# Kernel optimization log

Hardware: AMD Instinct MI355X
Metric: run time of the kernel (lower is better)

The kernel has to match this reference:

```python
import jax, jax.numpy as jnp
import numpy as np

# Config (matches init_kwargs)
T, B = 128, 32
I, H, O, G = 128, 320, 32, 8
GROUP = 16  # attn_group_size entries, 8 groups of 16 -> sums to I
DT, TAU_X, TAU_W = 0.02, 0.1, 0.2
ALPHA_X = DT / TAU_X          # 0.2
ALPHA_W = DT / TAU_W          # 0.1
E_PROP = 0.8


def _masks():
    e_h = int(E_PROP * H)  # 256
    # x2h: e_prop=1, zero_cols_prop=0, no diag removal -> all ones
    mask_x = jnp.ones((H, I), dtype=jnp.float32)
    # h2h: sign mask (+1 for E, -1 for I), diagonal zeroed
    sign_h = jnp.concatenate([jnp.ones(e_h), -jnp.ones(H - e_h)]).astype(jnp.float32)
    mask_h = jnp.tile(sign_h[None, :], (H, 1)) * (1.0 - jnp.eye(H, dtype=jnp.float32))
    # h2o: zero_cols = int(0.2*H) trailing columns removed, sign mask on the rest
    zc = int((1.0 - E_PROP) * H)  # 64
    exist = jnp.concatenate([jnp.ones(H - zc), jnp.zeros(zc)]).astype(jnp.float32)
    mask_o = jnp.tile((sign_h * exist)[None, :], (O, 1))
    # attn EILinear(H -> G): same column pattern as h2o
    mask_a = jnp.tile((sign_h * exist)[None, :], (G, 1))
    return mask_x, mask_h, mask_o, mask_a


def setup_inputs() -> dict:
    key = jax.random.key(0)
    ks = jax.random.split(key, 10)
    s = 0.05  # keep dynamics in a sane range
    return {
        "x": jax.random.normal(ks[0], (T, B, I), dtype=jnp.float32),
        "Rs": jax.random.uniform(ks[1], (T, B, 1), dtype=jnp.float32),
        "W_x2h": jax.random.normal(ks[2], (H, I), dtype=jnp.float32) * s,
        "W_h2h": jax.random.normal(ks[3], (H, H), dtype=jnp.float32) * s,
        "b_h2h": jax.random.normal(ks[4], (H,), dtype=jnp.float32) * s,
        "W_h2o": jax.random.normal(ks[5], (O, H), dtype=jnp.float32) * s,
        "b_h2o": jax.random.normal(ks[6], (O,), dtype=jnp.float32) * s,
        "W_attn": jax.random.normal(ks[7], (G, H), dtype=jnp.float32) * s,
        "b_attn": jax.random.normal(ks[8], (G,), dtype=jnp.float32) * s,
        "c_plas": jax.random.normal(ks[9], (6,), dtype=jnp.float32) * s,
    }


def reference(x, Rs, W_x2h, W_h2h, b_h2h, W_h2o, b_h2o, W_attn, b_attn, c_plas):
    mask_x, mask_h, mask_o, mask_a = _masks()
    relu = jax.nn.relu
    # effective (sign/existence constrained, positive) weights
    ew_attn = relu(W_attn) * mask_a                      # [G, H]
    ew_x0 = relu(W_x2h) * mask_x                         # [H, I]
    ew_h0 = relu(W_h2h) * mask_h                         # [H, H]
    c = jnp.abs(c_plas)

    state0 = jnp.zeros((B, H), dtype=x.dtype)            # x0=0, sigma_rec=0
    output0 = relu(state0)
    wx0 = jnp.broadcast_to(ew_x0[None], (B, H, I))       # batched fast weights
    wh0 = jnp.broadcast_to(ew_h0[None], (B, H, H))

    def step(carry, inp):
        state, output, wx, wh = carry
        x_t, R_t = inp                                   # [B,I], [B,1]
        # attention over hidden groups
        attn = jax.nn.softmax(output @ ew_attn.T + b_attn, axis=-1)  # [B,G]
        attn_full = jnp.repeat(attn, GROUP, axis=-1)     # [B,I]
        xm = x_t * attn_full * G
        # masked / positive-constrained fast weights applied per batch
        ewx = relu(wx) * mask_x[None]                    # [B,H,I]
        ewh = relu(wh) * mask_h[None]                    # [B,H,H]
        total = (jnp.einsum('bhi,bi->bh', ewx, xm)
                 + jnp.einsum('bhj,bj->bh', ewh, output) + b_h2h)
        new_state = state * (1.0 - ALPHA_X) + total * ALPHA_X
        new_output = jnp.tanh(relu(new_state))           # retanh
        # outer-product plasticity update
        R = R_t[:, :, None]                              # [B,1,1]
        wx_n = wx * (1.0 - ALPHA_W) + ALPHA_W * R * (
            c[0] * xm[:, None, :]
            + c[1] * new_output[:, :, None]
            + c[2] * jnp.einsum('bi,bj->bij', new_output, xm))
        wh_n = wh * (1.0 - ALPHA_W) + ALPHA_W * R * (
            c[3] * output[:, None, :]
            + c[4] * new_output[:, :, None]
            + c[5] * jnp.einsum('bi,bj->bij', new_output, output))
        return (new_state, new_output, wx_n, wh_n), new_output

    _, hs = jax.lax.scan(step, (state0, output0, wx0, wh0), (x, Rs))  # hs: [T,B,H]
    ew_o = relu(W_h2o) * mask_o                          # [O,H]
    out = jax.nn.sigmoid(jnp.einsum('tbh,oh->tbo', hs, ew_o) + b_h2o)
    return out, hs
```

## Files before the change

kernel.cpp:

```cpp
#include <hip/hip_runtime.h>

#define TT 128
#define BB 32
#define II 128
#define HH 320
#define OO 32
#define GG 8
#define HPAD 129

static __device__ __forceinline__ float fexp2(float x) { return __builtin_amdgcn_exp2f(x); }
static __device__ __forceinline__ float frcp(float x)  { return __builtin_amdgcn_rcpf(x); }

static __device__ __forceinline__ float tanh_pos(float x) {
    float e = fexp2(x * 2.8853900817779268f);
    return 1.0f - 2.0f * frcp(e + 1.0f);
}

__global__ __launch_bounds__(512, 2)
void leaky_rnn_kernel(const float* __restrict__ x, const float* __restrict__ Rs,
                      const float* __restrict__ Wx2h, const float* __restrict__ Wh2h,
                      const float* __restrict__ bh2h, const float* __restrict__ Wh2o,
                      const float* __restrict__ bh2o, const float* __restrict__ Wattn,
                      const float* __restrict__ battn, const float* __restrict__ cplas,
                      float* __restrict__ out, float* __restrict__ hs,
                      unsigned* __restrict__ ctr)
{
    const int tid  = threadIdx.x;
    const int bid  = blockIdx.x;
    const int b    = bid >> 3;
    const int sub  = bid & 7;
    const int w    = tid >> 6;
    const int lane = tid & 63;
    const int h0   = sub * 40;

    __shared__ float s_ea[GG * HH];
    __shared__ float s_out[HH];
    __shared__ float s_xm[II];
    __shared__ float s_logit[GG];
    __shared__ float s_hist[40 * HPAD];
    __shared__ float s_hs[16 * HH];

    for (int idx = tid; idx < GG * HH; idx += 512) {
        int h = idx % HH;
        float m = (h < 256) ? 1.f : (h == 256 ? -1.f : 0.f);
        s_ea[idx] = fmaxf(Wattn[idx], 0.f) * m;
    }
    if (tid < HH) s_out[tid] = 0.f;

    float wx[5][2], wh[5][5], st[5], bh[5];
    int hrow[5];
#pragma unroll
    for (int r = 0; r < 5; ++r) {
        int h = h0 + w * 5 + r;
        hrow[r] = h;
        bh[r] = bh2h[h];
        st[r] = 0.f;
#pragma unroll
        for (int c = 0; c < 2; ++c)
            wx[r][c] = fmaxf(Wx2h[h * II + lane + 64 * c], 0.f);
#pragma unroll
        for (int c = 0; c < 5; ++c) {
            int j = lane + 64 * c;
            float v = fmaxf(Wh2h[h * HH + j], 0.f);
            v = (c == 4) ? -v : v;
            wh[r][c] = (j == h) ? 0.f : v;
        }
    }
    float batt = battn[w];
    float c0 = fabsf(cplas[0]), c1 = fabsf(cplas[1]), c2 = fabsf(cplas[2]);
    float c3 = fabsf(cplas[3]), c4 = fabsf(cplas[4]), c5 = fabsf(cplas[5]);

    const float AX  = (float)(0.02 / 0.1);
    const float AW  = (float)(0.02 / 0.2);
    const float OMX = 1.f - AX;
    const float OMW = 1.f - AW;
    const float L2E = 1.4426950408889634f;

    __syncthreads();

    float xv_next = (tid < II) ? x[b * II + tid] : 0.f;

#pragma unroll 1
    for (int t = 0; t < TT; ++t) {
        float xv = xv_next;
        float Rv = Rs[t * BB + b];
        float A  = AW * Rv;

        float lp = 0.f;
#pragma unroll
        for (int k = 0; k < 5; ++k) {
            int hh2 = lane + 64 * k;
            lp = fmaf(s_ea[w * HH + hh2], s_out[hh2], lp);
        }
#pragma unroll
        for (int m = 1; m < 64; m <<= 1) lp += __shfl_xor(lp, m, 64);
        if (lane == 0) s_logit[w] = lp + batt;
        __syncthreads();

        if (tid < II) {
            float lg[8];
#pragma unroll
            for (int g = 0; g < 8; ++g) lg[g] = s_logit[g];
            float mx = lg[0];
#pragma unroll
            for (int g = 1; g < 8; ++g) mx = fmaxf(mx, lg[g]);
            float se = 0.f, eg[8];
#pragma unroll
            for (int g = 0; g < 8; ++g) { eg[g] = fexp2((lg[g] - mx) * L2E); se += eg[g]; }
            s_xm[tid] = xv * eg[tid >> 4] * 8.f * frcp(se);
        }
        __syncthreads();

        float xmc0 = s_xm[lane], xmc1 = s_xm[lane + 64];
        float oc[5];
#pragma unroll
        for (int c = 0; c < 5; ++c) oc[c] = s_out[lane + 64 * c];

        float no[5];
#pragma unroll
        for (int r = 0; r < 5; ++r) {
            int h = hrow[r];
            float p = fmaxf(wx[r][0], 0.f) * xmc0;
            p = fmaf(fmaxf(wx[r][1], 0.f), xmc1, p);
#pragma unroll
            for (int c = 0; c < 5; ++c) {
                float wv = fmaxf(wh[r][c], 0.f);
                float so = (c == 4) ? -oc[4] : oc[c];
                float term = wv * so;
                term = ((lane + 64 * c) == h) ? 0.f : term;
                p += term;
            }
#pragma unroll
            for (int m = 1; m < 64; m <<= 1) p += __shfl_xor(p, m, 64);
            float total = p + bh[r];
            st[r] = fmaf(st[r], OMX, total * AX);
            no[r] = tanh_pos(fmaxf(st[r], 0.f));
            if (lane == r) {
                __hip_atomic_store(&hs[(t * BB + b) * HH + h], no[r] + 2.0f,
                                   __ATOMIC_RELAXED, __HIP_MEMORY_SCOPE_AGENT);
                s_hist[(w * 5 + r) * HPAD + t] = no[r];
            }
        }

        if (t < TT - 1) {
            float Ac0 = A * c0, Ac1 = A * c1, Ac2 = A * c2;
            float Ac3 = A * c3, Ac4 = A * c4, Ac5 = A * c5;
#pragma unroll
            for (int r = 0; r < 5; ++r) {
                float u  = fmaf(Ac2, no[r], Ac0);
                float v  = Ac1 * no[r];
                float pp = fmaf(Ac5, no[r], Ac3);
                float qq = Ac4 * no[r];
                wx[r][0] = fmaf(wx[r][0], OMW, fmaf(u, xmc0, v));
                wx[r][1] = fmaf(wx[r][1], OMW, fmaf(u, xmc1, v));
#pragma unroll
                for (int c = 0; c < 5; ++c)
                    wh[r][c] = fmaf(wh[r][c], OMW, fmaf(pp, oc[c], qq));
            }
        }

        if (t + 1 < TT)
            xv_next = (tid < II) ? x[((t + 1) * BB + b) * II + tid] : 0.f;

        __syncthreads();

        if (t < TT - 1 && tid < HH) {
            float v;
            if (tid >= h0 && tid < h0 + 40) {
                v = s_hist[(tid - h0) * HPAD + t];
            } else {
                int guard = 0;
                do {
                    v = __hip_atomic_load(&hs[(t * BB + b) * HH + tid],
                                          __ATOMIC_RELAXED, __HIP_MEMORY_SCOPE_AGENT);
                    if (++guard > 2000000) break;
                } while (v < 1.0f);
                v -= 2.0f;
            }
            s_out[tid] = v;
        }
        __syncthreads();
    }

    if (tid == 0) {
        __hip_atomic_fetch_add(&ctr[b * 32], 1u, __ATOMIC_RELAXED, __HIP_MEMORY_SCOPE_AGENT);
        int guard = 0;
        while (__hip_atomic_load(&ctr[b * 32], __ATOMIC_RELAXED, __HIP_MEMORY_SCOPE_AGENT) < 8u) {
            if (++guard > 2000000) break;
            __builtin_amdgcn_s_sleep(1);
        }
    }
    __syncthreads();

    for (int idx = tid; idx < 16 * HH; idx += 512) {
        int tl = idx / HH, h = idx % HH;
        int t_g = sub * 16 + tl;
        s_hs[idx] = __hip_atomic_load(&hs[(t_g * BB + b) * HH + h],
                                      __ATOMIC_RELAXED, __HIP_MEMORY_SCOPE_AGENT) - 2.0f;
    }
    __syncthreads();
    {
        int t_loc = tid >> 5;
        int o     = tid & 31;
        int t_g   = sub * 16 + t_loc;
        const float* hp = &s_hs[t_loc * HH];
        float acc = bh2o[o];
#pragma unroll 4
        for (int h = 0; h < 257; ++h) {
            float m = (h == 256) ? -1.f : 1.f;
            acc = fmaf(fmaxf(Wh2o[o * HH + h], 0.f) * m, hp[h], acc);
        }
        float sg = frcp(1.f + fexp2(-acc * L2E));
        out[(t_g * BB + b) * OO + o] = sg;
    }

    __syncthreads();
    if (tid == 0) {
        __hip_atomic_fetch_add(&ctr[b * 32], 1u, __ATOMIC_RELAXED, __HIP_MEMORY_SCOPE_AGENT);
        int guard = 0;
        while (__hip_atomic_load(&ctr[b * 32], __ATOMIC_RELAXED, __HIP_MEMORY_SCOPE_AGENT) < 16u) {
            if (++guard > 2000000) break;
            __builtin_amdgcn_s_sleep(1);
        }
    }
    __syncthreads();

    for (int idx = tid; idx < 40 * TT; idx += 512) {
        int row = idx >> 7;
        int t   = idx & 127;
        __hip_atomic_store(&hs[(t * BB + b) * HH + h0 + row], s_hist[row * HPAD + t],
                           __ATOMIC_RELAXED, __HIP_MEMORY_SCOPE_AGENT);
    }
}

extern "C" void kernel_launch(void* const* d_in, const int* in_sizes, int n_in,
                              void* d_out, int out_size, void* d_ws, size_t ws_size,
                              hipStream_t stream) {
    const float* x     = (const float*)d_in[0];
    const float* Rs    = (const float*)d_in[1];
    const float* Wx2h  = (const float*)d_in[2];
    const float* Wh2h  = (const float*)d_in[3];
    const float* bh2h  = (const float*)d_in[4];
    const float* Wh2o  = (const float*)d_in[5];
    const float* bh2o  = (const float*)d_in[6];
    const float* Wattn = (const float*)d_in[7];
    const float* battn = (const float*)d_in[8];
    const float* cplas = (const float*)d_in[9];
    float* out = (float*)d_out;
    float* hs  = out + TT * BB * OO;
    unsigned* ctr = (unsigned*)d_ws;

    hipMemsetAsync(d_ws, 0, 32 * 32 * sizeof(unsigned), stream);
    hipLaunchKernelGGL(leaky_rnn_kernel, dim3(256), dim3(512), 0, stream,
                       x, Rs, Wx2h, Wh2h, bh2h, Wh2o, bh2o, Wattn, battn, cplas,
                       out, hs, ctr);
}
```

Baseline: 522.7 us.

## Detect same-XCC batch groups and use L2-local atomics for cross-block exchange

Block-to-batch mapping changes to b = bid & 31 so that, with round-robin XCC dispatch, the 8 blocks of one batch tend to land on the same XCC. A startup 64-bit counter barrier records each block's XCC ID. When all 8 blocks of a batch share an XCC, hidden-state publishing and polling use raw global_atomic_swap/or without the device-scope coherence path, which should cut the per-timestep cross-block latency. Correctness then rests on dispatch placement and on atomics being coherent within one XCC's L2. Spin guard limits are also lowered.

```diff
diff --git a/kernel.cpp b/kernel.cpp
--- a/kernel.cpp
+++ b/kernel.cpp
@@ -16,6 +16,22 @@
     return 1.0f - 2.0f * frcp(e + 1.0f);
 }
 
+static __device__ __forceinline__ void pub_store(float* p, float v, bool fast) {
+    if (fast)
+        asm volatile("global_atomic_swap %0, %1, off" :: "v"(p), "v"(v) : "memory");
+    else
+        __hip_atomic_store(p, v, __ATOMIC_RELAXED, __HIP_MEMORY_SCOPE_AGENT);
+}
+static __device__ __forceinline__ float gath_load(const float* p, bool fast) {
+    float v;
+    if (fast)
+        asm volatile("global_atomic_or %0, %1, %2, off sc0\n\ts_waitcnt vmcnt(0)"
+                     : "=&v"(v) : "v"(p), "v"(0) : "memory");
+    else
+        v = __hip_atomic_load(p, __ATOMIC_RELAXED, __HIP_MEMORY_SCOPE_AGENT);
+    return v;
+}
+
 __global__ __launch_bounds__(512, 2)
 void leaky_rnn_kernel(const float* __restrict__ x, const float* __restrict__ Rs,
                       const float* __restrict__ Wx2h, const float* __restrict__ Wh2h,
@@ -23,12 +39,12 @@
                       const float* __restrict__ bh2o, const float* __restrict__ Wattn,
                       const float* __restrict__ battn, const float* __restrict__ cplas,
                       float* __restrict__ out, float* __restrict__ hs,
-                      unsigned* __restrict__ ctr)
+                      unsigned* __restrict__ ctr, unsigned long long* __restrict__ bar64)
 {
     const int tid  = threadIdx.x;
     const int bid  = blockIdx.x;
-    const int b    = bid >> 3;
-    const int sub  = bid & 7;
+    const int b    = bid & 31;
+    const int sub  = bid >> 5;
     const int w    = tid >> 6;
     const int lane = tid & 63;
     const int h0   = sub * 40;
@@ -39,6 +55,23 @@
     __shared__ float s_logit[GG];
     __shared__ float s_hist[40 * HPAD];
     __shared__ float s_hs[16 * HH];
+    __shared__ int   s_fast;
+
+    unsigned xcc = 0;
+    asm volatile("s_getreg_b32 %0, hwreg(HW_REG_XCC_ID)" : "=s"(xcc));
+    if (tid == 0) {
+        unsigned long long add = 1ull | (1ull << (4 * (xcc + 1)));
+        __hip_atomic_fetch_add(&bar64[b * 16], add,
+                               __ATOMIC_RELAXED, __HIP_MEMORY_SCOPE_AGENT);
+        unsigned long long v;
+        int guard = 0;
+        do {
+            v = __hip_atomic_load(&bar64[b * 16],
+                                  __ATOMIC_RELAXED, __HIP_MEMORY_SCOPE_AGENT);
+            if (++guard > 5000000) break;
+        } while ((v & 0xFull) != 8ull);
+        s_fast = (((v >> (4 * (xcc + 1))) & 0xFull) == 8ull);
+    }
 
     for (int idx = tid; idx < GG * HH; idx += 512) {
         int h = idx % HH;
@@ -77,6 +110,7 @@
     const float L2E = 1.4426950408889634f;
 
     __syncthreads();
+    const bool fast = (s_fast != 0);
 
     float xv_next = (tid < II) ? x[b * II + tid] : 0.f;
 
@@ -115,6 +149,7 @@
         float oc[5];
 #pragma unroll
         for (int c = 0; c < 5; ++c) oc[c] = s_out[lane + 64 * c];
+        float oc4n = -oc[4];
 
         float no[5];
 #pragma unroll
@@ -125,7 +160,7 @@
 #pragma unroll
             for (int c = 0; c < 5; ++c) {
                 float wv = fmaxf(wh[r][c], 0.f);
-                float so = (c == 4) ? -oc[4] : oc[c];
+                float so = (c == 4) ? oc4n : oc[c];
                 float term = wv * so;
                 term = ((lane + 64 * c) == h) ? 0.f : term;
                 p += term;
@@ -136,8 +171,7 @@
             st[r] = fmaf(st[r], OMX, total * AX);
             no[r] = tanh_pos(fmaxf(st[r], 0.f));
             if (lane == r) {
-                __hip_atomic_store(&hs[(t * BB + b) * HH + h], no[r] + 2.0f,
-                                   __ATOMIC_RELAXED, __HIP_MEMORY_SCOPE_AGENT);
+                pub_store(&hs[(t * BB + b) * HH + h], no[r] + 2.0f, fast);
                 s_hist[(w * 5 + r) * HPAD + t] = no[r];
             }
         }
@@ -171,9 +205,8 @@
             } else {
                 int guard = 0;
                 do {
-                    v = __hip_atomic_load(&hs[(t * BB + b) * HH + tid],
-                                          __ATOMIC_RELAXED, __HIP_MEMORY_SCOPE_AGENT);
-                    if (++guard > 2000000) break;
+                    v = gath_load(&hs[(t * BB + b) * HH + tid], fast);
+                    if (++guard > 300000) break;
                 } while (v < 1.0f);
                 v -= 2.0f;
             }
@@ -186,7 +219,7 @@
         __hip_atomic_fetch_add(&ctr[b * 32], 1u, __ATOMIC_RELAXED, __HIP_MEMORY_SCOPE_AGENT);
         int guard = 0;
         while (__hip_atomic_load(&ctr[b * 32], __ATOMIC_RELAXED, __HIP_MEMORY_SCOPE_AGENT) < 8u) {
-            if (++guard > 2000000) break;
+            if (++guard > 1000000) break;
             __builtin_amdgcn_s_sleep(1);
         }
     }
@@ -195,8 +228,7 @@
     for (int idx = tid; idx < 16 * HH; idx += 512) {
         int tl = idx / HH, h = idx % HH;
         int t_g = sub * 16 + tl;
-        s_hs[idx] = __hip_atomic_load(&hs[(t_g * BB + b) * HH + h],
-                                      __ATOMIC_RELAXED, __HIP_MEMORY_SCOPE_AGENT) - 2.0f;
+        s_hs[idx] = gath_load(&hs[(t_g * BB + b) * HH + h], fast) - 2.0f;
     }
     __syncthreads();
     {
@@ -219,7 +251,7 @@
         __hip_atomic_fetch_add(&ctr[b * 32], 1u, __ATOMIC_RELAXED, __HIP_MEMORY_SCOPE_AGENT);
         int guard = 0;
         while (__hip_atomic_load(&ctr[b * 32], __ATOMIC_RELAXED, __HIP_MEMORY_SCOPE_AGENT) < 16u) {
-            if (++guard > 2000000) break;
+            if (++guard > 1000000) break;
             __builtin_amdgcn_s_sleep(1);
         }
     }
@@ -228,8 +260,7 @@
     for (int idx = tid; idx < 40 * TT; idx += 512) {
         int row = idx >> 7;
         int t   = idx & 127;
-        __hip_atomic_store(&hs[(t * BB + b) * HH + h0 + row], s_hist[row * HPAD + t],
-                           __ATOMIC_RELAXED, __HIP_MEMORY_SCOPE_AGENT);
+        pub_store(&hs[(t * BB + b) * HH + h0 + row], s_hist[row * HPAD + t], fast);
     }
 }
 
@@ -249,9 +280,10 @@
     float* out = (float*)d_out;
     float* hs  = out + TT * BB * OO;
     unsigned* ctr = (unsigned*)d_ws;
-
-    hipMemsetAsync(d_ws, 0, 32 * 32 * sizeof(unsigned), stream);
+    unsigned long long* bar64 = (unsigned long long*)((char*)d_ws + 32 * 32 * sizeof(unsigned));
+
+    hipMemsetAsync(d_ws, 0, 32 * 32 * sizeof(unsigned) + 32 * 16 * sizeof(unsigned long long), stream);
     hipLaunchKernelGGL(leaky_rnn_kernel, dim3(256), dim3(512), 0, stream,
                        x, Rs, Wx2h, Wh2h, bh2h, Wh2o, bh2o, Wattn, battn, cplas,
-                       out, hs, ctr);
-}
+                       out, hs, ctr, bar64);
+}
```

Result: slower. 559.6 us (+7.1%).

## Process two batch elements per block to interleave independent recurrences

Applied to the files above, without the earlier changes.

Each block now advances two independent batch recurrences (b and b+16) side by side, and the grid shrinks from 256 to 128 blocks. The aim is to spread the per-step barrier and cross-block polling cost over twice the useful work, and to overlap the two chains' latency. Attention weights now live in registers, and every thread computes the softmax itself, which drops one __syncthreads per step. Diagonal masking moves into the weight init (set to -1e30, which relu zeroes), removing a per-term select. The cost is doubled plasticity-weight registers under a 512-thread, 2-blocks-per-CU launch bound, which risks register spills and more serial work per block.

```diff
diff --git a/kernel.cpp b/kernel.cpp
--- a/kernel.cpp
+++ b/kernel.cpp
@@ -14,6 +14,13 @@
 static __device__ __forceinline__ float tanh_pos(float x) {
     float e = fexp2(x * 2.8853900817779268f);
     return 1.0f - 2.0f * frcp(e + 1.0f);
+}
+
+static __device__ __forceinline__ void pub_store(float* p, float v) {
+    __hip_atomic_store(p, v, __ATOMIC_RELAXED, __HIP_MEMORY_SCOPE_AGENT);
+}
+static __device__ __forceinline__ float gath_load(const float* p) {
+    return __hip_atomic_load(p, __ATOMIC_RELAXED, __HIP_MEMORY_SCOPE_AGENT);
 }
 
 __global__ __launch_bounds__(512, 2)
@@ -26,199 +33,245 @@
                       unsigned* __restrict__ ctr)
 {
     const int tid  = threadIdx.x;
-    const int bid  = blockIdx.x;
-    const int b    = bid >> 3;
-    const int sub  = bid & 7;
+    const int q    = blockIdx.x;
+    const int bA   = q & 15;
+    const int bB   = bA + 16;
+    const int sub  = q >> 4;
     const int w    = tid >> 6;
     const int lane = tid & 63;
     const int h0   = sub * 40;
 
-    __shared__ float s_ea[GG * HH];
-    __shared__ float s_out[HH];
-    __shared__ float s_xm[II];
-    __shared__ float s_logit[GG];
-    __shared__ float s_hist[40 * HPAD];
+    __shared__ float s_outA[HH], s_outB[HH];
+    __shared__ float s_logitA[GG], s_logitB[GG];
+    __shared__ float s_histA[40 * HPAD];
+    __shared__ float s_histB[40 * HPAD];
     __shared__ float s_hs[16 * HH];
 
-    for (int idx = tid; idx < GG * HH; idx += 512) {
-        int h = idx % HH;
-        float m = (h < 256) ? 1.f : (h == 256 ? -1.f : 0.f);
-        s_ea[idx] = fmaxf(Wattn[idx], 0.f) * m;
-    }
-    if (tid < HH) s_out[tid] = 0.f;
-
-    float wx[5][2], wh[5][5], st[5], bh[5];
+    float ea[5];
+#pragma unroll
+    for (int k = 0; k < 5; ++k) {
+        int j = lane + 64 * k;
+        float m = (j < 256) ? 1.f : (j == 256 ? -1.f : 0.f);
+        ea[k] = fmaxf(Wattn[w * HH + j], 0.f) * m;
+    }
+    if (tid < HH) { s_outA[tid] = 0.f; s_outB[tid] = 0.f; }
+
+    float wxA[5][2], whA[5][5], wxB[5][2], whB[5][5];
+    float stA[5], stB[5], bh[5];
     int hrow[5];
 #pragma unroll
     for (int r = 0; r < 5; ++r) {
         int h = h0 + w * 5 + r;
-        hrow[r] = h;
-        bh[r] = bh2h[h];
-        st[r] = 0.f;
-#pragma unroll
-        for (int c = 0; c < 2; ++c)
-            wx[r][c] = fmaxf(Wx2h[h * II + lane + 64 * c], 0.f);
+        hrow[r] = h; bh[r] = bh2h[h]; stA[r] = 0.f; stB[r] = 0.f;
+#pragma unroll
+        for (int c = 0; c < 2; ++c) {
+            float v = fmaxf(Wx2h[h * II + lane + 64 * c], 0.f);
+            wxA[r][c] = v; wxB[r][c] = v;
+        }
 #pragma unroll
         for (int c = 0; c < 5; ++c) {
             int j = lane + 64 * c;
             float v = fmaxf(Wh2h[h * HH + j], 0.f);
             v = (c == 4) ? -v : v;
-            wh[r][c] = (j == h) ? 0.f : v;
+            v = (j == h) ? -1e30f : v;
+            whA[r][c] = v; whB[r][c] = v;
         }
     }
     float batt = battn[w];
     float c0 = fabsf(cplas[0]), c1 = fabsf(cplas[1]), c2 = fabsf(cplas[2]);
     float c3 = fabsf(cplas[3]), c4 = fabsf(cplas[4]), c5 = fabsf(cplas[5]);
-
-    const float AX  = (float)(0.02 / 0.1);
-    const float AW  = (float)(0.02 / 0.2);
-    const float OMX = 1.f - AX;
-    const float OMW = 1.f - AW;
+    const float AX = 0.2f, OMX = 0.8f, AW = 0.1f, OMW = 0.9f;
     const float L2E = 1.4426950408889634f;
+    const int g0 = lane >> 4;
 
     __syncthreads();
 
-    float xv_next = (tid < II) ? x[b * II + tid] : 0.f;
+    float xA0 = x[bA * II + lane], xA1 = x[bA * II + lane + 64];
+    float xB0 = x[bB * II + lane], xB1 = x[bB * II + lane + 64];
+    float RvA = Rs[bA], RvB = Rs[bB];
 
 #pragma unroll 1
     for (int t = 0; t < TT; ++t) {
-        float xv = xv_next;
-        float Rv = Rs[t * BB + b];
-        float A  = AW * Rv;
-
-        float lp = 0.f;
+        float lpA = 0.f, lpB = 0.f;
 #pragma unroll
         for (int k = 0; k < 5; ++k) {
-            int hh2 = lane + 64 * k;
-            lp = fmaf(s_ea[w * HH + hh2], s_out[hh2], lp);
-        }
-#pragma unroll
-        for (int m = 1; m < 64; m <<= 1) lp += __shfl_xor(lp, m, 64);
-        if (lane == 0) s_logit[w] = lp + batt;
-        __syncthreads();
-
-        if (tid < II) {
+            lpA = fmaf(ea[k], s_outA[lane + 64 * k], lpA);
+            lpB = fmaf(ea[k], s_outB[lane + 64 * k], lpB);
+        }
+#pragma unroll
+        for (int m = 1; m < 64; m <<= 1) {
+            lpA += __shfl_xor(lpA, m, 64);
+            lpB += __shfl_xor(lpB, m, 64);
+        }
+        if (lane == 0) { s_logitA[w] = lpA + batt; s_logitB[w] = lpB + batt; }
+        __syncthreads();
+
+        float noA[5], ocA[5], xmA0, xmA1;
+        float noB[5], ocB[5], xmB0, xmB1;
+
+        {
             float lg[8];
 #pragma unroll
-            for (int g = 0; g < 8; ++g) lg[g] = s_logit[g];
+            for (int g = 0; g < 8; ++g) lg[g] = s_logitA[g];
             float mx = lg[0];
 #pragma unroll
             for (int g = 1; g < 8; ++g) mx = fmaxf(mx, lg[g]);
             float se = 0.f, eg[8];
 #pragma unroll
             for (int g = 0; g < 8; ++g) { eg[g] = fexp2((lg[g] - mx) * L2E); se += eg[g]; }
-            s_xm[tid] = xv * eg[tid >> 4] * 8.f * frcp(se);
-        }
-        __syncthreads();
-
-        float xmc0 = s_xm[lane], xmc1 = s_xm[lane + 64];
-        float oc[5];
-#pragma unroll
-        for (int c = 0; c < 5; ++c) oc[c] = s_out[lane + 64 * c];
-
-        float no[5];
-#pragma unroll
-        for (int r = 0; r < 5; ++r) {
-            int h = hrow[r];
-            float p = fmaxf(wx[r][0], 0.f) * xmc0;
-            p = fmaf(fmaxf(wx[r][1], 0.f), xmc1, p);
-#pragma unroll
-            for (int c = 0; c < 5; ++c) {
-                float wv = fmaxf(wh[r][c], 0.f);
-                float so = (c == 4) ? -oc[4] : oc[c];
-                float term = wv * so;
-                term = ((lane + 64 * c) == h) ? 0.f : term;
-                p += term;
-            }
-#pragma unroll
-            for (int m = 1; m < 64; m <<= 1) p += __shfl_xor(p, m, 64);
-            float total = p + bh[r];
-            st[r] = fmaf(st[r], OMX, total * AX);
-            no[r] = tanh_pos(fmaxf(st[r], 0.f));
-            if (lane == r) {
-                __hip_atomic_store(&hs[(t * BB + b) * HH + h], no[r] + 2.0f,
-                                   __ATOMIC_RELAXED, __HIP_MEMORY_SCOPE_AGENT);
-                s_hist[(w * 5 + r) * HPAD + t] = no[r];
+            float k8 = 8.f * frcp(se);
+            xmA0 = xA0 * eg[g0] * k8;  xmA1 = xA1 * eg[g0 + 4] * k8;
+#pragma unroll
+            for (int c = 0; c < 5; ++c) ocA[c] = s_outA[lane + 64 * c];
+            float oc4n = -ocA[4];
+#pragma unroll
+            for (int r = 0; r < 5; ++r) {
+                float p = fmaxf(wxA[r][0], 0.f) * xmA0;
+                p = fmaf(fmaxf(wxA[r][1], 0.f), xmA1, p);
+#pragma unroll
+                for (int c = 0; c < 5; ++c) {
+                    float so = (c == 4) ? oc4n : ocA[c];
+                    p = fmaf(fmaxf(whA[r][c], 0.f), so, p);
+                }
+#pragma unroll
+                for (int m = 1; m < 64; m <<= 1) p += __shfl_xor(p, m, 64);
+                stA[r] = fmaf(stA[r], OMX, (p + bh[r]) * AX);
+                noA[r] = tanh_pos(fmaxf(stA[r], 0.f));
+                if (lane == r) {
+                    pub_store(&hs[(t * BB + bA) * HH + hrow[r]], noA[r] + 2.0f);
+                    s_histA[(w * 5 + r) * HPAD + t] = noA[r];
+                }
+            }
+        }
+        {
+            float lg[8];
+#pragma unroll
+            for (int g = 0; g < 8; ++g) lg[g] = s_logitB[g];
+            float mx = lg[0];
+#pragma unroll
+            for (int g = 1; g < 8; ++g) mx = fmaxf(mx, lg[g]);
+            float se = 0.f, eg[8];
+#pragma unroll
+            for (int g = 0; g < 8; ++g) { eg[g] = fexp2((lg[g] - mx) * L2E); se += eg[g]; }
+            float k8 = 8.f * frcp(se);
+            xmB0 = xB0 * eg[g0] * k8;  xmB1 = xB1 * eg[g0 + 4] * k8;
+#pragma unroll
+            for (int c = 0; c < 5; ++c) ocB[c] = s_outB[lane + 64 * c];
+            float oc4n = -ocB[4];
+#pragma unroll
+            for (int r = 0; r < 5; ++r) {
+                float p = fmaxf(wxB[r][0], 0.f) * xmB0;
+                p = fmaf(fmaxf(wxB[r][1], 0.f), xmB1, p);
+#pragma unroll
+                for (int c = 0; c < 5; ++c) {
+                    float so = (c == 4) ? oc4n : ocB[c];
+                    p = fmaf(fmaxf(whB[r][c], 0.f), so, p);
+                }
+#pragma unroll
+                for (int m = 1; m < 64; m <<= 1) p += __shfl_xor(p, m, 64);
+                stB[r] = fmaf(stB[r], OMX, (p + bh[r]) * AX);
+                noB[r] = tanh_pos(fmaxf(stB[r], 0.f));
+                if (lane == r) {
+                    pub_store(&hs[(t * BB + bB) * HH + hrow[r]], noB[r] + 2.0f);
+                    s_histB[(w * 5 + r) * HPAD + t] = noB[r];
+                }
             }
         }
 
         if (t < TT - 1) {
-            float Ac0 = A * c0, Ac1 = A * c1, Ac2 = A * c2;
-            float Ac3 = A * c3, Ac4 = A * c4, Ac5 = A * c5;
+            float A_ = AW * RvA;
+            float a0 = A_*c0, a1 = A_*c1, a2 = A_*c2, a3 = A_*c3, a4 = A_*c4, a5 = A_*c5;
 #pragma unroll
             for (int r = 0; r < 5; ++r) {
-                float u  = fmaf(Ac2, no[r], Ac0);
-                float v  = Ac1 * no[r];
-                float pp = fmaf(Ac5, no[r], Ac3);
-                float qq = Ac4 * no[r];
-                wx[r][0] = fmaf(wx[r][0], OMW, fmaf(u, xmc0, v));
-                wx[r][1] = fmaf(wx[r][1], OMW, fmaf(u, xmc1, v));
+                float u = fmaf(a2, noA[r], a0), v = a1 * noA[r];
+                float pp = fmaf(a5, noA[r], a3), qq = a4 * noA[r];
+                wxA[r][0] = fmaf(wxA[r][0], OMW, fmaf(u, xmA0, v));
+                wxA[r][1] = fmaf(wxA[r][1], OMW, fmaf(u, xmA1, v));
 #pragma unroll
                 for (int c = 0; c < 5; ++c)
-                    wh[r][c] = fmaf(wh[r][c], OMW, fmaf(pp, oc[c], qq));
-            }
-        }
-
-        if (t + 1 < TT)
-            xv_next = (tid < II) ? x[((t + 1) * BB + b) * II + tid] : 0.f;
+                    whA[r][c] = fmaf(whA[r][c], OMW, fmaf(pp, ocA[c], qq));
+            }
+            float B_ = AW * RvB;
+            float e0 = B_*c0, e1 = B_*c1, e2 = B_*c2, e3 = B_*c3, e4 = B_*c4, e5 = B_*c5;
+#pragma unroll
+            for (int r = 0; r < 5; ++r) {
+                float u = fmaf(e2, noB[r], e0), v = e1 * noB[r];
+                float pp = fmaf(e5, noB[r], e3), qq = e4 * noB[r];
+                wxB[r][0] = fmaf(wxB[r][0], OMW, fmaf(u, xmB0, v));
+                wxB[r][1] = fmaf(wxB[r][1], OMW, fmaf(u, xmB1, v));
+#pragma unroll
+                for (int c = 0; c < 5; ++c)
+                    whB[r][c] = fmaf(whB[r][c], OMW, fmaf(pp, ocB[c], qq));
+            }
+            int tn = t + 1;
+            xA0 = x[(tn * BB + bA) * II + lane]; xA1 = x[(tn * BB + bA) * II + lane + 64];
+            xB0 = x[(tn * BB + bB) * II + lane]; xB1 = x[(tn * BB + bB) * II + lane + 64];
+            RvA = Rs[tn * BB + bA]; RvB = Rs[tn * BB + bB];
+        }
 
         __syncthreads();
 
         if (t < TT - 1 && tid < HH) {
-            float v;
+            float vA, vB;
             if (tid >= h0 && tid < h0 + 40) {
-                v = s_hist[(tid - h0) * HPAD + t];
+                vA = s_histA[(tid - h0) * HPAD + t];
+                vB = s_histB[(tid - h0) * HPAD + t];
             } else {
+                const float* pA = &hs[(t * BB + bA) * HH + tid];
+                const float* pB = &hs[(t * BB + bB) * HH + tid];
+                vA = gath_load(pA); vB = gath_load(pB);
                 int guard = 0;
-                do {
-                    v = __hip_atomic_load(&hs[(t * BB + b) * HH + tid],
-                                          __ATOMIC_RELAXED, __HIP_MEMORY_SCOPE_AGENT);
-                    if (++guard > 2000000) break;
-                } while (v < 1.0f);
-                v -= 2.0f;
-            }
-            s_out[tid] = v;
+                while (vA < 1.f || vB < 1.f) {
+                    if (vA < 1.f) vA = gath_load(pA);
+                    if (vB < 1.f) vB = gath_load(pB);
+                    if (++guard > 300000) break;
+                }
+                vA -= 2.f; vB -= 2.f;
+            }
+            s_outA[tid] = vA; s_outB[tid] = vB;
         }
         __syncthreads();
     }
 
     if (tid == 0) {
-        __hip_atomic_fetch_add(&ctr[b * 32], 1u, __ATOMIC_RELAXED, __HIP_MEMORY_SCOPE_AGENT);
+        __hip_atomic_fetch_add(&ctr[bA * 32], 1u, __ATOMIC_RELAXED, __HIP_MEMORY_SCOPE_AGENT);
         int guard = 0;
-        while (__hip_atomic_load(&ctr[b * 32], __ATOMIC_RELAXED, __HIP_MEMORY_SCOPE_AGENT) < 8u) {
+        while (__hip_atomic_load(&ctr[bA * 32], __ATOMIC_RELAXED, __HIP_MEMORY_SCOPE_AGENT) < 8u) {
             if (++guard > 2000000) break;
             __builtin_amdgcn_s_sleep(1);
         }
     }
     __syncthreads();
 
-    for (int idx = tid; idx < 16 * HH; idx += 512) {
-        int tl = idx / HH, h = idx % HH;
-        int t_g = sub * 16 + tl;
-        s_hs[idx] = __hip_atomic_load(&hs[(t_g * BB + b) * HH + h],
-                                      __ATOMIC_RELAXED, __HIP_MEMORY_SCOPE_AGENT) - 2.0f;
-    }
-    __syncthreads();
-    {
-        int t_loc = tid >> 5;
-        int o     = tid & 31;
-        int t_g   = sub * 16 + t_loc;
-        const float* hp = &s_hs[t_loc * HH];
-        float acc = bh2o[o];
+#pragma unroll 1
+    for (int pass = 0; pass < 2; ++pass) {
+        int b = pass ? bB : bA;
+        for (int idx = tid; idx < 16 * HH; idx += 512) {
+            int tl = idx / HH, h = idx % HH;
+            int t_g = sub * 16 + tl;
+            s_hs[idx] = gath_load(&hs[(t_g * BB + b) * HH + h]) - 2.0f;
+        }
+        __syncthreads();
+        {
+            int t_loc = tid >> 5;
+            int o     = tid & 31;
+            int t_g   = sub * 16 + t_loc;
+            const float* hp = &s_hs[t_loc * HH];
+            float acc = bh2o[o];
 #pragma unroll 4
-        for (int h = 0; h < 257; ++h) {
-            float m = (h == 256) ? -1.f : 1.f;
-            acc = fmaf(fmaxf(Wh2o[o * HH + h], 0.f) * m, hp[h], acc);
-        }
-        float sg = frcp(1.f + fexp2(-acc * L2E));
-        out[(t_g * BB + b) * OO + o] = sg;
-    }
-
-    __syncthreads();
+            for (int h = 0; h < 257; ++h) {
+                float m = (h == 256) ? -1.f : 1.f;
+                acc = fmaf(fmaxf(Wh2o[o * HH + h], 0.f) * m, hp[h], acc);
+            }
+            out[(t_g * BB + b) * OO + o] = frcp(1.f + fexp2(-acc * L2E));
+        }
+        __syncthreads();
+    }
+
     if (tid == 0) {
-        __hip_atomic_fetch_add(&ctr[b * 32], 1u, __ATOMIC_RELAXED, __HIP_MEMORY_SCOPE_AGENT);
+        __hip_atomic_fetch_add(&ctr[bA * 32], 1u, __ATOMIC_RELAXED, __HIP_MEMORY_SCOPE_AGENT);
         int guard = 0;
-        while (__hip_atomic_load(&ctr[b * 32], __ATOMIC_RELAXED, __HIP_MEMORY_SCOPE_AGENT) < 16u) {
+        while (__hip_atomic_load(&ctr[bA * 32], __ATOMIC_RELAXED, __HIP_MEMORY_SCOPE_AGENT) < 16u) {
             if (++guard > 2000000) break;
             __builtin_amdgcn_s_sleep(1);
         }
@@ -228,8 +281,8 @@
     for (int idx = tid; idx < 40 * TT; idx += 512) {
         int row = idx >> 7;
         int t   = idx & 127;
-        __hip_atomic_store(&hs[(t * BB + b) * HH + h0 + row], s_hist[row * HPAD + t],
-                           __ATOMIC_RELAXED, __HIP_MEMORY_SCOPE_AGENT);
+        pub_store(&hs[(t * BB + bA) * HH + h0 + row], s_histA[row * HPAD + t]);
+        pub_store(&hs[(t * BB + bB) * HH + h0 + row], s_histB[row * HPAD + t]);
     }
 }
 
@@ -250,8 +303,8 @@
     float* hs  = out + TT * BB * OO;
     unsigned* ctr = (unsigned*)d_ws;
 
-    hipMemsetAsync(d_ws, 0, 32 * 32 * sizeof(unsigned), stream);
-    hipLaunchKernelGGL(leaky_rnn_kernel, dim3(256), dim3(512), 0, stream,
+    (void)hipMemsetAsync(d_ws, 0, 32 * 32 * sizeof(unsigned), stream);
+    hipLaunchKernelGGL(leaky_rnn_kernel, dim3(128), dim3(512), 0, stream,
                        x, Rs, Wx2h, Wh2h, bh2h, Wh2o, bh2o, Wattn, battn, cplas,
                        out, hs, ctr);
 }
```

After: 794.7 us. +52.0%, slower.
